# Kernel optimization log

Measured on AMD Instinct MI355X. Metric: run time of the kernel, lower is better.

Reference implementation:

```python
import jax, jax.numpy as jnp
import numpy as np

TEMPERATURE = 2.718281828459045  # math.e
N_EXPERTS = 64
N_ACTIVE = 44  # int(64 * 0.7)
EPS = 1e-08


def setup_inputs() -> dict:
    key = jax.random.key(0)
    k1, k2 = jax.random.split(key)
    B, S, D = 4, 4096, 2048
    x = jax.random.normal(k1, (B, S, D), dtype=jnp.float32)
    # xavier_uniform for Linear(D, E): bound = sqrt(6 / (D + E))
    bound = float(np.sqrt(6.0 / (D + N_EXPERTS)))
    gate_w = jax.random.uniform(k2, (N_EXPERTS, D), dtype=jnp.float32,
                                minval=-bound, maxval=bound)
    return {"x": x, "gate_w": gate_w}


def reference(x, gate_w):
    B, S, D = x.shape
    E = gate_w.shape[0]
    # gate + temperature
    scores = jnp.einsum("bsd,ed->bse", x, gate_w) / TEMPERATURE
    probs = jax.nn.softmax(scores, axis=-1)  # (B, S, E)
    topk_vals, topk_idx = jax.lax.top_k(probs, N_ACTIVE)  # (B, S, K)
    # scatter 1.0 into mask at top-k indices (flatten token dims)
    flat_idx = topk_idx.reshape(-1, N_ACTIVE)  # (N, K)
    rows = jnp.arange(flat_idx.shape[0])[:, None]  # (N, 1)
    mask = jnp.zeros((flat_idx.shape[0], E), dtype=probs.dtype)
    mask = mask.at[rows, flat_idx].set(1.0).reshape(B, S, E)
    weights = probs * mask
    weights = weights / (jnp.sum(weights, axis=-1, keepdims=True) + EPS)
    return weights
```

## Files before the change

kernel.cpp:

```cpp
#include <hip/hip_runtime.h>


#define NTOK   16384
#define DIM    2048
#define NEXP   64
#define NACT   44
#define BM     32
#define BK     64
#define NSTEP  (DIM / BK)
#define GAP_EPS 2e-4f

typedef __attribute__((ext_vector_type(4))) float f4;
typedef __attribute__((ext_vector_type(8))) short bf8;
typedef __attribute__((ext_vector_type(4))) float f32x4;

union BF8U { unsigned u[4]; bf8 v; };

__device__ __forceinline__ unsigned bf16rn(float f) {
  unsigned u = __float_as_uint(f);
  return (u + 0x7fffu + ((u >> 16) & 1u)) >> 16;
}

__device__ __forceinline__ void split8t(f4 a, f4 b, bf8& hi, bf8& lo) {
  float fa[8] = {a.x, a.y, a.z, a.w, b.x, b.y, b.z, b.w};
  BF8U h, l;
  #pragma unroll
  for (int j = 0; j < 4; ++j) {
    const float f0 = fa[2 * j], f1 = fa[2 * j + 1];
    const unsigned u0 = __float_as_uint(f0), u1 = __float_as_uint(f1);
    const unsigned h0 = u0 & 0xffff0000u, h1 = u1 & 0xffff0000u;
    h.u[j] = (u0 >> 16) | h1;
    const float l0 = f0 - __uint_as_float(h0);
    const float l1 = f1 - __uint_as_float(h1);
    l.u[j] = bf16rn(l0) | (bf16rn(l1) << 16);
  }
  hi = h.v; lo = l.v;
}

__device__ __forceinline__ float wave_max(float v) {
  #pragma unroll
  for (int j = 32; j > 0; j >>= 1) v = fmaxf(v, __shfl_xor(v, j, 64));
  return v;
}
__device__ __forceinline__ float wave_sum(float v) {
  #pragma unroll
  for (int j = 32; j > 0; j >>= 1) v += __shfl_xor(v, j, 64);
  return v;
}

__global__ __launch_bounds__(256, 2) void boltzmann_router_kernel(
    const float* __restrict__ x, const float* __restrict__ gw,
    float* __restrict__ out) {
  __shared__ unsigned short whi[2][NEXP * BK];
  __shared__ unsigned short wlo[2][NEXP * BK];

  const int t    = threadIdx.x;
  const int ln   = t & 63;
  const int wv   = t >> 6;
  const int tw   = wv >> 1;
  const int nh   = wv & 1;
  const int tok0 = blockIdx.x * BM;

  const int wexp = t >> 2;
  const int wko  = (t & 3) * 16;
  const int ws0  = (t & 3) * 2;
  const int we7  = wexp & 7;

  const int xrow = tok0 + tw * 16 + (ln & 15);
  const int xk   = (ln >> 4) * 8;

  f4 xbuf[4], wbuf[4];
  bf8 ahi[2], alo[2];

  auto issue_loads = [&](int step) {
    const float* xp = x + (size_t)xrow * DIM + step * BK + xk;
    xbuf[0] = *(const f4*)(xp);
    xbuf[1] = *(const f4*)(xp + 4);
    xbuf[2] = *(const f4*)(xp + 32);
    xbuf[3] = *(const f4*)(xp + 36);
    const float* wp = gw + (size_t)wexp * DIM + step * BK + wko;
    wbuf[0] = *(const f4*)(wp);
    wbuf[1] = *(const f4*)(wp + 4);
    wbuf[2] = *(const f4*)(wp + 8);
    wbuf[3] = *(const f4*)(wp + 12);
  };
  auto convert_store = [&](int buf) {
    split8t(xbuf[0], xbuf[1], ahi[0], alo[0]);
    split8t(xbuf[2], xbuf[3], ahi[1], alo[1]);
    bf8 h0, l0, h1, l1;
    split8t(wbuf[0], wbuf[1], h0, l0);
    split8t(wbuf[2], wbuf[3], h1, l1);
    const int p0 = ((ws0 ^ we7) * 8), p1 = (((ws0 + 1) ^ we7) * 8);
    *reinterpret_cast<bf8*>(&whi[buf][wexp * 64 + p0]) = h0;
    *reinterpret_cast<bf8*>(&whi[buf][wexp * 64 + p1]) = h1;
    *reinterpret_cast<bf8*>(&wlo[buf][wexp * 64 + p0]) = l0;
    *reinterpret_cast<bf8*>(&wlo[buf][wexp * 64 + p1]) = l1;
  };

  issue_loads(0);
  convert_store(0);
  __syncthreads();

  f32x4 acc[2] = {};
  for (int step = 0; step < NSTEP; ++step) {
    const int cur = step & 1;
    if (step + 1 < NSTEP) issue_loads(step + 1);
    #pragma unroll
    for (int h = 0; h < 2; ++h) {
      #pragma unroll
      for (int nf = 0; nf < 2; ++nf) {
        const int ee  = nh * 32 + nf * 16 + (ln & 15);
        const int ps  = ((h * 4 + (ln >> 4)) ^ (ln & 7)) * 8;
        const int idx = ee * 64 + ps;
        const bf8 bh = *reinterpret_cast<const bf8*>(&whi[cur][idx]);
        const bf8 bl = *reinterpret_cast<const bf8*>(&wlo[cur][idx]);
        acc[nf] = __builtin_amdgcn_mfma_f32_16x16x32_bf16(ahi[h], bh, acc[nf], 0, 0, 0);
        acc[nf] = __builtin_amdgcn_mfma_f32_16x16x32_bf16(alo[h], bh, acc[nf], 0, 0, 0);
        acc[nf] = __builtin_amdgcn_mfma_f32_16x16x32_bf16(ahi[h], bl, acc[nf], 0, 0, 0);
      }
    }
    if (step + 1 < NSTEP) convert_store(cur ^ 1);
    __syncthreads();
  }

  float* sc = reinterpret_cast<float*>(&whi[0][0]);
  const float INVT = 0.36787944117144233f;
  #pragma unroll
  for (int nf = 0; nf < 2; ++nf) {
    #pragma unroll
    for (int r = 0; r < 4; ++r) {
      const int tokr = tw * 16 + (ln >> 4) * 4 + r;
      const int expc = nh * 32 + nf * 16 + (ln & 15);
      sc[tokr * 65 + expc] = acc[nf][r] * INVT;
    }
  }
  __syncthreads();

  #pragma unroll 1
  for (int it = 0; it < 8; ++it) {
    const int m   = wv * 8 + it;
    const int tok = tok0 + m;
    const float s = sc[m * 65 + ln];

    float v = s;
    #pragma unroll
    for (int k = 2; k <= 64; k <<= 1) {
      #pragma unroll
      for (int j = k >> 1; j > 0; j >>= 1) {
        const float o  = __shfl_xor(v, j, 64);
        const bool up  = ((ln & k) == 0);
        const bool lo_ = ((ln & j) == 0);
        v = (lo_ == up) ? fminf(v, o) : fmaxf(v, o);
      }
    }
    const float v20 = __shfl(v, 64 - NACT, 64);
    const float v19 = __shfl(v, 64 - NACT - 1, 64);

    bool sel;
    float sv = s;
    if (v20 - v19 < GAP_EPS) {
      const f4* xr = reinterpret_cast<const f4*>(x + (size_t)tok * DIM);
      const f4* wr = reinterpret_cast<const f4*>(gw + (size_t)ln * DIM);
      double p0=0,p1=0,p2=0,p3=0,p4=0,p5=0,p6=0,p7=0;
      for (int k = 0; k < DIM / 8; ++k) {
        const f4 xa = xr[2*k], xb = xr[2*k+1];
        const f4 wa = wr[2*k], wb = wr[2*k+1];
        p0 = fma((double)xa.x, (double)wa.x, p0);
        p1 = fma((double)xa.y, (double)wa.y, p1);
        p2 = fma((double)xa.z, (double)wa.z, p2);
        p3 = fma((double)xa.w, (double)wa.w, p3);
        p4 = fma((double)xb.x, (double)wb.x, p4);
        p5 = fma((double)xb.y, (double)wb.y, p5);
        p6 = fma((double)xb.z, (double)wb.z, p6);
        p7 = fma((double)xb.w, (double)wb.w, p7);
      }
      const double s64 =
          (((p0+p1)+(p2+p3)) + ((p4+p5)+(p6+p7))) * 0.36787944117144233;
      double dv = s64;
      #pragma unroll
      for (int k = 2; k <= 64; k <<= 1) {
        #pragma unroll
        for (int j = k >> 1; j > 0; j >>= 1) {
          const double o = __shfl_xor(dv, j, 64);
          const bool up  = ((ln & k) == 0);
          const bool lo_ = ((ln & j) == 0);
          dv = (lo_ == up) ? fmin(dv, o) : fmax(dv, o);
        }
      }
      const double thr64 = __shfl(dv, 64 - NACT, 64);
      sel = (s64 >= thr64);
      sv = (float)s64;
    } else {
      sel = (s >= v20);
    }

    const float mx  = wave_max(sv);
    const float ex  = __expf(sv - mx);
    const float sum = wave_sum(ex);
    const float p   = ex / sum;
    const float ps  = wave_sum(sel ? p : 0.0f);
    out[(size_t)tok * NEXP + ln] = sel ? (p / (ps + 1e-8f)) : 0.0f;
  }
}

extern "C" void kernel_launch(void* const* d_in, const int* in_sizes, int n_in,
                              void* d_out, int out_size, void* d_ws, size_t ws_size,
                              hipStream_t stream) {
  const float* x  = (const float*)d_in[0];
  const float* gw = (const float*)d_in[1];
  float* out = (float*)d_out;
  boltzmann_router_kernel<<<dim3(NTOK / BM), dim3(256), 0, stream>>>(x, gw, out);
}
```

Baseline: 308.6 us.

## Pre-split gate weights and triple-buffer direct-to-LDS async loads

Adds a small pre-kernel that splits the gate weights into swizzled bf16 hi/lo planes in workspace once per call. The main kernel grows to 64-token tiles with 512 threads and streams x and the pre-split weights straight into LDS through global_load_lds, three stages deep, with manual vmcnt waits. This takes the per-block weight conversion and register staging out of the loop and overlaps loads with MFMA. In exchange it adds a second launch, uses more LDS per block so fewer blocks fit per CU, and relies on hand-written waitcnt counts being correct.

```diff
diff --git a/kernel.cpp b/kernel.cpp
--- a/kernel.cpp
+++ b/kernel.cpp
@@ -1,13 +1,13 @@
 #include <hip/hip_runtime.h>
 
 
-#define NTOK   16384
-#define DIM    2048
-#define NEXP   64
-#define NACT   44
-#define BM     32
-#define BK     64
-#define NSTEP  (DIM / BK)
+#define NTOK  16384
+#define DIM   2048
+#define NEXP  64
+#define NACT  44
+#define BM    64
+#define BK    64
+#define NSTEP (DIM / BK)
 #define GAP_EPS 2e-4f
 
 typedef __attribute__((ext_vector_type(4))) float f4;
@@ -48,88 +48,134 @@
   return v;
 }
 
-__global__ __launch_bounds__(256, 2) void boltzmann_router_kernel(
+__global__ __launch_bounds__(256) void split_w_kernel(
+    const float* __restrict__ gw, unsigned short* __restrict__ whi_g,
+    unsigned short* __restrict__ wlo_g) {
+  const int i  = blockIdx.x * 256 + threadIdx.x;
+  const int s  = i >> 9;
+  const int r  = (i >> 3) & 63;
+  const int ls = i & 7;
+  const int gs = ls ^ (r & 7);
+  const float* src = gw + (size_t)r * DIM + s * BK + gs * 8;
+  const f4 a = *reinterpret_cast<const f4*>(src);
+  const f4 b = *reinterpret_cast<const f4*>(src + 4);
+  bf8 hi, lo;
+  split8t(a, b, hi, lo);
+  *reinterpret_cast<bf8*>(whi_g + (size_t)i * 8) = hi;
+  *reinterpret_cast<bf8*>(wlo_g + (size_t)i * 8) = lo;
+}
+
+__global__ __launch_bounds__(512, 1) void boltzmann_router_kernel(
     const float* __restrict__ x, const float* __restrict__ gw,
-    float* __restrict__ out) {
-  __shared__ unsigned short whi[2][NEXP * BK];
-  __shared__ unsigned short wlo[2][NEXP * BK];
+    const unsigned short* __restrict__ whi_g,
+    const unsigned short* __restrict__ wlo_g, float* __restrict__ out) {
+  __shared__ alignas(16) float          xlds[3][BM * BK];
+  __shared__ alignas(16) unsigned short whilds[3][NEXP * BK];
+  __shared__ alignas(16) unsigned short wlolds[3][NEXP * BK];
 
   const int t    = threadIdx.x;
   const int ln   = t & 63;
   const int wv   = t >> 6;
-  const int tw   = wv >> 1;
+  const int tq   = wv >> 1;
   const int nh   = wv & 1;
   const int tok0 = blockIdx.x * BM;
 
-  const int wexp = t >> 2;
-  const int wko  = (t & 3) * 16;
-  const int ws0  = (t & 3) * 2;
-  const int we7  = wexp & 7;
-
-  const int xrow = tok0 + tw * 16 + (ln & 15);
-  const int xk   = (ln >> 4) * 8;
-
-  f4 xbuf[4], wbuf[4];
-  bf8 ahi[2], alo[2];
-
-  auto issue_loads = [&](int step) {
-    const float* xp = x + (size_t)xrow * DIM + step * BK + xk;
-    xbuf[0] = *(const f4*)(xp);
-    xbuf[1] = *(const f4*)(xp + 4);
-    xbuf[2] = *(const f4*)(xp + 32);
-    xbuf[3] = *(const f4*)(xp + 36);
-    const float* wp = gw + (size_t)wexp * DIM + step * BK + wko;
-    wbuf[0] = *(const f4*)(wp);
-    wbuf[1] = *(const f4*)(wp + 4);
-    wbuf[2] = *(const f4*)(wp + 8);
-    wbuf[3] = *(const f4*)(wp + 12);
+  size_t gsrc[4];
+  if (wv < 4) {
+    #pragma unroll
+    for (int i = 0; i < 4; ++i) {
+      const int c  = wv * 4 + i;
+      const int r  = 4 * c + (ln >> 4);
+      const int gs = (ln & 15) ^ (r & 15);
+      gsrc[i] = (size_t)(tok0 + r) * DIM + gs * 4;
+    }
+  } else {
+    const int base = ((wv - 4) & 1) * 4;
+    #pragma unroll
+    for (int i = 0; i < 4; ++i) {
+      const int c2 = base + i;
+      gsrc[i] = (size_t)c2 * 512 + ln * 8;
+    }
+  }
+
+  auto STAGE = [&](int buf, int step) {
+    if (wv < 4) {
+      #pragma unroll
+      for (int i = 0; i < 4; ++i) {
+        const int c = wv * 4 + i;
+        __builtin_amdgcn_global_load_lds(
+            (const __attribute__((address_space(1))) void*)(x + gsrc[i] + (size_t)step * BK),
+            (__attribute__((address_space(3))) void*)&xlds[buf][c * 256], 16, 0, 0);
+      }
+    } else if (wv < 6) {
+      #pragma unroll
+      for (int i = 0; i < 4; ++i) {
+        const int c2 = (wv - 4) * 4 + i;
+        __builtin_amdgcn_global_load_lds(
+            (const __attribute__((address_space(1))) void*)(whi_g + gsrc[i] + (size_t)step * 4096),
+            (__attribute__((address_space(3))) void*)&whilds[buf][c2 * 512], 16, 0, 0);
+      }
+    } else {
+      #pragma unroll
+      for (int i = 0; i < 4; ++i) {
+        const int c2 = (wv - 6) * 4 + i;
+        __builtin_amdgcn_global_load_lds(
+            (const __attribute__((address_space(1))) void*)(wlo_g + gsrc[i] + (size_t)step * 4096),
+            (__attribute__((address_space(3))) void*)&wlolds[buf][c2 * 512], 16, 0, 0);
+      }
+    }
   };
-  auto convert_store = [&](int buf) {
-    split8t(xbuf[0], xbuf[1], ahi[0], alo[0]);
-    split8t(xbuf[2], xbuf[3], ahi[1], alo[1]);
-    bf8 h0, l0, h1, l1;
-    split8t(wbuf[0], wbuf[1], h0, l0);
-    split8t(wbuf[2], wbuf[3], h1, l1);
-    const int p0 = ((ws0 ^ we7) * 8), p1 = (((ws0 + 1) ^ we7) * 8);
-    *reinterpret_cast<bf8*>(&whi[buf][wexp * 64 + p0]) = h0;
-    *reinterpret_cast<bf8*>(&whi[buf][wexp * 64 + p1]) = h1;
-    *reinterpret_cast<bf8*>(&wlo[buf][wexp * 64 + p0]) = l0;
-    *reinterpret_cast<bf8*>(&wlo[buf][wexp * 64 + p1]) = l1;
-  };
-
-  issue_loads(0);
-  convert_store(0);
-  __syncthreads();
-
+
+  STAGE(0, 0);
+  STAGE(1, 1);
+  STAGE(2, 2);
+
+  const int arow = tq * 16 + (ln & 15);
   f32x4 acc[2] = {};
+
+  int cur = 0;
   for (int step = 0; step < NSTEP; ++step) {
-    const int cur = step & 1;
-    if (step + 1 < NSTEP) issue_loads(step + 1);
-    #pragma unroll
-    for (int h = 0; h < 2; ++h) {
-      #pragma unroll
-      for (int nf = 0; nf < 2; ++nf) {
-        const int ee  = nh * 32 + nf * 16 + (ln & 15);
-        const int ps  = ((h * 4 + (ln >> 4)) ^ (ln & 7)) * 8;
-        const int idx = ee * 64 + ps;
-        const bf8 bh = *reinterpret_cast<const bf8*>(&whi[cur][idx]);
-        const bf8 bl = *reinterpret_cast<const bf8*>(&wlo[cur][idx]);
-        acc[nf] = __builtin_amdgcn_mfma_f32_16x16x32_bf16(ahi[h], bh, acc[nf], 0, 0, 0);
-        acc[nf] = __builtin_amdgcn_mfma_f32_16x16x32_bf16(alo[h], bh, acc[nf], 0, 0, 0);
-        acc[nf] = __builtin_amdgcn_mfma_f32_16x16x32_bf16(ahi[h], bl, acc[nf], 0, 0, 0);
-      }
-    }
-    if (step + 1 < NSTEP) convert_store(cur ^ 1);
-    __syncthreads();
-  }
-
-  float* sc = reinterpret_cast<float*>(&whi[0][0]);
+    if (step < NSTEP - 2)       asm volatile("s_waitcnt vmcnt(8)" ::: "memory");
+    else if (step == NSTEP - 2) asm volatile("s_waitcnt vmcnt(4)" ::: "memory");
+    else                        asm volatile("s_waitcnt vmcnt(0)" ::: "memory");
+    __builtin_amdgcn_s_barrier();
+
+    bf8 ahi[2], alo[2];
+    #pragma unroll
+    for (int ks = 0; ks < 2; ++ks) {
+      const int gs0 = ks * 8 + (ln >> 4) * 2;
+      const int ls0 = gs0 ^ (arow & 15);
+      const int ls1 = (gs0 + 1) ^ (arow & 15);
+      const f4 a0 = *reinterpret_cast<const f4*>(&xlds[cur][arow * 64 + ls0 * 4]);
+      const f4 a1 = *reinterpret_cast<const f4*>(&xlds[cur][arow * 64 + ls1 * 4]);
+      split8t(a0, a1, ahi[ks], alo[ks]);
+    }
+    #pragma unroll
+    for (int nf = 0; nf < 2; ++nf) {
+      const int e = nh * 32 + nf * 16 + (ln & 15);
+      #pragma unroll
+      for (int ks = 0; ks < 2; ++ks) {
+        const int gs = ks * 4 + (ln >> 4);
+        const int ls = gs ^ (e & 7);
+        const bf8 bh = *reinterpret_cast<const bf8*>(&whilds[cur][e * 64 + ls * 8]);
+        const bf8 bl = *reinterpret_cast<const bf8*>(&wlolds[cur][e * 64 + ls * 8]);
+        acc[nf] = __builtin_amdgcn_mfma_f32_16x16x32_bf16(ahi[ks], bh, acc[nf], 0, 0, 0);
+        acc[nf] = __builtin_amdgcn_mfma_f32_16x16x32_bf16(alo[ks], bh, acc[nf], 0, 0, 0);
+        acc[nf] = __builtin_amdgcn_mfma_f32_16x16x32_bf16(ahi[ks], bl, acc[nf], 0, 0, 0);
+      }
+    }
+    __builtin_amdgcn_s_barrier();
+    if (step + 3 < NSTEP) STAGE(cur, step + 3);
+    cur = (cur == 2) ? 0 : cur + 1;
+  }
+
+  float* sc = reinterpret_cast<float*>(&xlds[0][0]);
   const float INVT = 0.36787944117144233f;
   #pragma unroll
   for (int nf = 0; nf < 2; ++nf) {
     #pragma unroll
     for (int r = 0; r < 4; ++r) {
-      const int tokr = tw * 16 + (ln >> 4) * 4 + r;
+      const int tokr = tq * 16 + (ln >> 4) * 4 + r;
       const int expc = nh * 32 + nf * 16 + (ln & 15);
       sc[tokr * 65 + expc] = acc[nf][r] * INVT;
     }
@@ -209,5 +255,9 @@
   const float* x  = (const float*)d_in[0];
   const float* gw = (const float*)d_in[1];
   float* out = (float*)d_out;
-  boltzmann_router_kernel<<<dim3(NTOK / BM), dim3(256), 0, stream>>>(x, gw, out);
-}
+  unsigned short* whi_g = (unsigned short*)d_ws;
+  unsigned short* wlo_g = whi_g + (size_t)NEXP * DIM;
+  split_w_kernel<<<dim3(64), dim3(256), 0, stream>>>(gw, whi_g, wlo_g);
+  boltzmann_router_kernel<<<dim3(NTOK / BM), dim3(512), 0, stream>>>(
+      x, gw, whi_g, wlo_g, out);
+}
```

Measured after the change: 281.1 us. 1.1x faster.

## Pre-split gate weights into bf16 hi/lo image and stream via global_load_lds

Applied to the files above, without the earlier changes.

Adds a prologue kernel that splits the gate weights into swizzled bf16 hi/lo planes once per call in workspace. The main kernel then copies those planes directly into LDS with global_load_lds in large double-buffered stages, instead of converting weights per block every K-step. Each block now handles 64 tokens with one wave owning 16 tokens and all 64 experts, and x is prefetched several steps ahead. The post-processing handles two tokens per iteration to interleave shuffles. The cost is a second launch, 128KB of LDS per block limiting occupancy to one block per CU, and only 256 blocks in the grid.

```diff
diff --git a/kernel.cpp b/kernel.cpp
--- a/kernel.cpp
+++ b/kernel.cpp
@@ -1,13 +1,10 @@
 #include <hip/hip_runtime.h>
 
 
-#define NTOK   16384
-#define DIM    2048
-#define NEXP   64
-#define NACT   44
-#define BM     32
-#define BK     64
-#define NSTEP  (DIM / BK)
+#define NTOK  16384
+#define DIM   2048
+#define NEXP  64
+#define NACT  44
 #define GAP_EPS 2e-4f
 
 typedef __attribute__((ext_vector_type(4))) float f4;
@@ -48,158 +45,185 @@
   return v;
 }
 
-__global__ __launch_bounds__(256, 2) void boltzmann_router_kernel(
+__device__ void fixup_token(const float* __restrict__ x,
+                            const float* __restrict__ gw, int tok, int ln,
+                            bool& sel, float& sv) {
+  const f4* xr = reinterpret_cast<const f4*>(x + (size_t)tok * DIM);
+  const f4* wr = reinterpret_cast<const f4*>(gw + (size_t)ln * DIM);
+  double p0=0,p1=0,p2=0,p3=0,p4=0,p5=0,p6=0,p7=0;
+  for (int k = 0; k < DIM / 8; ++k) {
+    const f4 xa = xr[2*k], xb = xr[2*k+1];
+    const f4 wa = wr[2*k], wb = wr[2*k+1];
+    p0 = fma((double)xa.x, (double)wa.x, p0);
+    p1 = fma((double)xa.y, (double)wa.y, p1);
+    p2 = fma((double)xa.z, (double)wa.z, p2);
+    p3 = fma((double)xa.w, (double)wa.w, p3);
+    p4 = fma((double)xb.x, (double)wb.x, p4);
+    p5 = fma((double)xb.y, (double)wb.y, p5);
+    p6 = fma((double)xb.z, (double)wb.z, p6);
+    p7 = fma((double)xb.w, (double)wb.w, p7);
+  }
+  const double s64 =
+      (((p0+p1)+(p2+p3)) + ((p4+p5)+(p6+p7))) * 0.36787944117144233;
+  double dv = s64;
+  #pragma unroll
+  for (int k = 2; k <= 64; k <<= 1) {
+    #pragma unroll
+    for (int j = k >> 1; j > 0; j >>= 1) {
+      const double o = __shfl_xor(dv, j, 64);
+      const bool up  = ((ln & k) == 0);
+      const bool lo_ = ((ln & j) == 0);
+      dv = (lo_ == up) ? fmin(dv, o) : fmax(dv, o);
+    }
+  }
+  const double thr64 = __shfl(dv, 64 - NACT, 64);
+  sel = (s64 >= thr64);
+  sv = (float)s64;
+}
+
+__global__ __launch_bounds__(256) void split_w_kernel(
+    const float* __restrict__ gw, unsigned short* __restrict__ img) {
+  const int id  = blockIdx.x * 256 + threadIdx.x;
+  const int s   = id >> 11;
+  const int rem = id & 2047;
+  const int e   = rem >> 5;
+  const int l   = rem & 31;
+  const float* src = gw + (size_t)e * DIM + s * 256 + l * 8;
+  const f4 a = *reinterpret_cast<const f4*>(src);
+  const f4 b = *reinterpret_cast<const f4*>(src + 4);
+  bf8 hi, lo;
+  split8t(a, b, hi, lo);
+  const int phys = l ^ (e & 7);
+  unsigned short* d = img + (size_t)s * 32768 + (e * 32 + phys) * 8;
+  *reinterpret_cast<bf8*>(d)         = hi;
+  *reinterpret_cast<bf8*>(d + 16384) = lo;
+}
+
+__global__ __launch_bounds__(256, 1) void boltzmann_router_kernel(
     const float* __restrict__ x, const float* __restrict__ gw,
-    float* __restrict__ out) {
-  __shared__ unsigned short whi[2][NEXP * BK];
-  __shared__ unsigned short wlo[2][NEXP * BK];
+    const unsigned short* __restrict__ img, float* __restrict__ out) {
+  __shared__ alignas(16) unsigned short wbuf[2][32768];
+  __shared__ float sc[4][16 * 65];
 
   const int t    = threadIdx.x;
   const int ln   = t & 63;
   const int wv   = t >> 6;
-  const int tw   = wv >> 1;
-  const int nh   = wv & 1;
-  const int tok0 = blockIdx.x * BM;
-
-  const int wexp = t >> 2;
-  const int wko  = (t & 3) * 16;
-  const int ws0  = (t & 3) * 2;
-  const int we7  = wexp & 7;
-
-  const int xrow = tok0 + tw * 16 + (ln & 15);
-  const int xk   = (ln >> 4) * 8;
-
-  f4 xbuf[4], wbuf[4];
-  bf8 ahi[2], alo[2];
-
-  auto issue_loads = [&](int step) {
-    const float* xp = x + (size_t)xrow * DIM + step * BK + xk;
-    xbuf[0] = *(const f4*)(xp);
-    xbuf[1] = *(const f4*)(xp + 4);
-    xbuf[2] = *(const f4*)(xp + 32);
-    xbuf[3] = *(const f4*)(xp + 36);
-    const float* wp = gw + (size_t)wexp * DIM + step * BK + wko;
-    wbuf[0] = *(const f4*)(wp);
-    wbuf[1] = *(const f4*)(wp + 4);
-    wbuf[2] = *(const f4*)(wp + 8);
-    wbuf[3] = *(const f4*)(wp + 12);
+  const int tok0 = blockIdx.x * 64;
+
+  auto STAGE = [&](int b, int sub) {
+    const unsigned short* src = img + (size_t)sub * 32768;
+    #pragma unroll
+    for (int i = 0; i < 16; ++i) {
+      const int chunk = i * 256 + wv * 64;
+      __builtin_amdgcn_global_load_lds(
+          (const __attribute__((address_space(1))) void*)(src + (size_t)(chunk + ln) * 8),
+          (__attribute__((address_space(3))) void*)&wbuf[b][chunk * 8], 16, 0, 0);
+    }
   };
-  auto convert_store = [&](int buf) {
-    split8t(xbuf[0], xbuf[1], ahi[0], alo[0]);
-    split8t(xbuf[2], xbuf[3], ahi[1], alo[1]);
-    bf8 h0, l0, h1, l1;
-    split8t(wbuf[0], wbuf[1], h0, l0);
-    split8t(wbuf[2], wbuf[3], h1, l1);
-    const int p0 = ((ws0 ^ we7) * 8), p1 = (((ws0 + 1) ^ we7) * 8);
-    *reinterpret_cast<bf8*>(&whi[buf][wexp * 64 + p0]) = h0;
-    *reinterpret_cast<bf8*>(&whi[buf][wexp * 64 + p1]) = h1;
-    *reinterpret_cast<bf8*>(&wlo[buf][wexp * 64 + p0]) = l0;
-    *reinterpret_cast<bf8*>(&wlo[buf][wexp * 64 + p1]) = l1;
-  };
-
-  issue_loads(0);
-  convert_store(0);
-  __syncthreads();
-
-  f32x4 acc[2] = {};
-  for (int step = 0; step < NSTEP; ++step) {
-    const int cur = step & 1;
-    if (step + 1 < NSTEP) issue_loads(step + 1);
-    #pragma unroll
-    for (int h = 0; h < 2; ++h) {
+
+  const int xrow = tok0 + wv * 16 + (ln & 15);
+  const float* xb = x + (size_t)xrow * DIM + (ln >> 4) * 8;
+
+  f4 xqa[4], xqb[4];
+
+  STAGE(0, 0);
+  __builtin_amdgcn_sched_barrier(0);
+  #pragma unroll
+  for (int s = 0; s < 4; ++s) {
+    xqa[s] = *reinterpret_cast<const f4*>(xb + s * 32);
+    xqb[s] = *reinterpret_cast<const f4*>(xb + s * 32 + 4);
+  }
+  asm volatile("s_waitcnt vmcnt(8)" ::: "memory");
+  __builtin_amdgcn_s_barrier();
+
+  f32x4 acc[4] = {};
+
+  #pragma unroll 1
+  for (int sub = 0; sub < 8; ++sub) {
+    const int cur = sub & 1;
+    if (sub < 7) {
+      STAGE(cur ^ 1, sub + 1);
+      __builtin_amdgcn_sched_barrier(0);
+    }
+    #pragma unroll
+    for (int kq = 0; kq < 8; ++kq) {
+      const int S = sub * 8 + kq;
+      bf8 ahi, alo;
+      split8t(xqa[kq & 3], xqb[kq & 3], ahi, alo);
+      if (S + 4 < 64) {
+        xqa[kq & 3] = *reinterpret_cast<const f4*>(xb + (S + 4) * 32);
+        xqb[kq & 3] = *reinterpret_cast<const f4*>(xb + (S + 4) * 32 + 4);
+      }
       #pragma unroll
-      for (int nf = 0; nf < 2; ++nf) {
-        const int ee  = nh * 32 + nf * 16 + (ln & 15);
-        const int ps  = ((h * 4 + (ln >> 4)) ^ (ln & 7)) * 8;
-        const int idx = ee * 64 + ps;
-        const bf8 bh = *reinterpret_cast<const bf8*>(&whi[cur][idx]);
-        const bf8 bl = *reinterpret_cast<const bf8*>(&wlo[cur][idx]);
-        acc[nf] = __builtin_amdgcn_mfma_f32_16x16x32_bf16(ahi[h], bh, acc[nf], 0, 0, 0);
-        acc[nf] = __builtin_amdgcn_mfma_f32_16x16x32_bf16(alo[h], bh, acc[nf], 0, 0, 0);
-        acc[nf] = __builtin_amdgcn_mfma_f32_16x16x32_bf16(ahi[h], bl, acc[nf], 0, 0, 0);
+      for (int nf = 0; nf < 4; ++nf) {
+        const int e    = nf * 16 + (ln & 15);
+        const int phys = (kq * 4 + (ln >> 4)) ^ (e & 7);
+        const int idx  = (e * 32 + phys) * 8;
+        const bf8 bh = *reinterpret_cast<const bf8*>(&wbuf[cur][idx]);
+        const bf8 bl = *reinterpret_cast<const bf8*>(&wbuf[cur][16384 + idx]);
+        acc[nf] = __builtin_amdgcn_mfma_f32_16x16x32_bf16(ahi, bh, acc[nf], 0, 0, 0);
+        acc[nf] = __builtin_amdgcn_mfma_f32_16x16x32_bf16(alo, bh, acc[nf], 0, 0, 0);
+        acc[nf] = __builtin_amdgcn_mfma_f32_16x16x32_bf16(ahi, bl, acc[nf], 0, 0, 0);
       }
     }
-    if (step + 1 < NSTEP) convert_store(cur ^ 1);
-    __syncthreads();
-  }
-
-  float* sc = reinterpret_cast<float*>(&whi[0][0]);
+    if (sub < 7) {
+      asm volatile("s_waitcnt vmcnt(8)" ::: "memory");
+      __builtin_amdgcn_s_barrier();
+    }
+  }
+
   const float INVT = 0.36787944117144233f;
   #pragma unroll
-  for (int nf = 0; nf < 2; ++nf) {
+  for (int nf = 0; nf < 4; ++nf) {
     #pragma unroll
     for (int r = 0; r < 4; ++r) {
-      const int tokr = tw * 16 + (ln >> 4) * 4 + r;
-      const int expc = nh * 32 + nf * 16 + (ln & 15);
-      sc[tokr * 65 + expc] = acc[nf][r] * INVT;
-    }
-  }
-  __syncthreads();
+      const int tr = (ln >> 4) * 4 + r;
+      const int ec = nf * 16 + (ln & 15);
+      sc[wv][tr * 65 + ec] = acc[nf][r] * INVT;
+    }
+  }
 
   #pragma unroll 1
   for (int it = 0; it < 8; ++it) {
-    const int m   = wv * 8 + it;
-    const int tok = tok0 + m;
-    const float s = sc[m * 65 + ln];
-
-    float v = s;
+    const int m0 = 2 * it, m1 = 2 * it + 1;
+    const float s0 = sc[wv][m0 * 65 + ln];
+    const float s1 = sc[wv][m1 * 65 + ln];
+
+    float v0 = s0, v1 = s1;
     #pragma unroll
     for (int k = 2; k <= 64; k <<= 1) {
       #pragma unroll
       for (int j = k >> 1; j > 0; j >>= 1) {
-        const float o  = __shfl_xor(v, j, 64);
+        const float o0 = __shfl_xor(v0, j, 64);
+        const float o1 = __shfl_xor(v1, j, 64);
         const bool up  = ((ln & k) == 0);
         const bool lo_ = ((ln & j) == 0);
-        v = (lo_ == up) ? fminf(v, o) : fmaxf(v, o);
+        v0 = (lo_ == up) ? fminf(v0, o0) : fmaxf(v0, o0);
+        v1 = (lo_ == up) ? fminf(v1, o1) : fmaxf(v1, o1);
       }
     }
-    const float v20 = __shfl(v, 64 - NACT, 64);
-    const float v19 = __shfl(v, 64 - NACT - 1, 64);
-
-    bool sel;
-    float sv = s;
-    if (v20 - v19 < GAP_EPS) {
-      const f4* xr = reinterpret_cast<const f4*>(x + (size_t)tok * DIM);
-      const f4* wr = reinterpret_cast<const f4*>(gw + (size_t)ln * DIM);
-      double p0=0,p1=0,p2=0,p3=0,p4=0,p5=0,p6=0,p7=0;
-      for (int k = 0; k < DIM / 8; ++k) {
-        const f4 xa = xr[2*k], xb = xr[2*k+1];
-        const f4 wa = wr[2*k], wb = wr[2*k+1];
-        p0 = fma((double)xa.x, (double)wa.x, p0);
-        p1 = fma((double)xa.y, (double)wa.y, p1);
-        p2 = fma((double)xa.z, (double)wa.z, p2);
-        p3 = fma((double)xa.w, (double)wa.w, p3);
-        p4 = fma((double)xb.x, (double)wb.x, p4);
-        p5 = fma((double)xb.y, (double)wb.y, p5);
-        p6 = fma((double)xb.z, (double)wb.z, p6);
-        p7 = fma((double)xb.w, (double)wb.w, p7);
-      }
-      const double s64 =
-          (((p0+p1)+(p2+p3)) + ((p4+p5)+(p6+p7))) * 0.36787944117144233;
-      double dv = s64;
-      #pragma unroll
-      for (int k = 2; k <= 64; k <<= 1) {
-        #pragma unroll
-        for (int j = k >> 1; j > 0; j >>= 1) {
-          const double o = __shfl_xor(dv, j, 64);
-          const bool up  = ((ln & k) == 0);
-          const bool lo_ = ((ln & j) == 0);
-          dv = (lo_ == up) ? fmin(dv, o) : fmax(dv, o);
-        }
-      }
-      const double thr64 = __shfl(dv, 64 - NACT, 64);
-      sel = (s64 >= thr64);
-      sv = (float)s64;
-    } else {
-      sel = (s >= v20);
-    }
-
-    const float mx  = wave_max(sv);
-    const float ex  = __expf(sv - mx);
-    const float sum = wave_sum(ex);
-    const float p   = ex / sum;
-    const float ps  = wave_sum(sel ? p : 0.0f);
-    out[(size_t)tok * NEXP + ln] = sel ? (p / (ps + 1e-8f)) : 0.0f;
+    const float v20_0 = __shfl(v0, 64 - NACT, 64);
+    const float v19_0 = __shfl(v0, 64 - NACT - 1, 64);
+    const float v20_1 = __shfl(v1, 64 - NACT, 64);
+    const float v19_1 = __shfl(v1, 64 - NACT - 1, 64);
+
+    const int tokA = tok0 + wv * 16 + m0;
+    const int tokB = tok0 + wv * 16 + m1;
+
+    bool selA, selB;
+    float svA = s0, svB = s1;
+    if (v20_0 - v19_0 < GAP_EPS) fixup_token(x, gw, tokA, ln, selA, svA);
+    else                         selA = (s0 >= v20_0);
+    if (v20_1 - v19_1 < GAP_EPS) fixup_token(x, gw, tokB, ln, selB, svB);
+    else                         selB = (s1 >= v20_1);
+
+    const float mxA = wave_max(svA),            mxB = wave_max(svB);
+    const float exA = __expf(svA - mxA),        exB = __expf(svB - mxB);
+    const float smA = wave_sum(exA),            smB = wave_sum(exB);
+    const float pA  = exA / smA,                pB  = exB / smB;
+    const float psA = wave_sum(selA ? pA : 0.f), psB = wave_sum(selB ? pB : 0.f);
+    out[(size_t)tokA * NEXP + ln] = selA ? (pA / (psA + 1e-8f)) : 0.0f;
+    out[(size_t)tokB * NEXP + ln] = selB ? (pB / (psB + 1e-8f)) : 0.0f;
   }
 }
 
@@ -209,5 +233,8 @@
   const float* x  = (const float*)d_in[0];
   const float* gw = (const float*)d_in[1];
   float* out = (float*)d_out;
-  boltzmann_router_kernel<<<dim3(NTOK / BM), dim3(256), 0, stream>>>(x, gw, out);
-}
+  unsigned short* img = (unsigned short*)d_ws;
+  split_w_kernel<<<dim3(64), dim3(256), 0, stream>>>(gw, img);
+  boltzmann_router_kernel<<<dim3(NTOK / 64), dim3(256), 0, stream>>>(
+      x, gw, img, out);
+}
```

Measured after the change: 318.1 us. +3.1%, slower.
